# Kernel optimization log

Hardware: AMD Instinct MI355X
Metric: run time of the kernel (lower is better)

The kernel has to match this reference:

```python
import jax, jax.numpy as jnp
import numpy as np

N_NODES = 100000
IN_DIM = 512
OUT_DIM = 16
N_EDGES = 3200000


def setup_inputs() -> dict:
    key = jax.random.key(0)
    k1, k2, k3, k4 = jax.random.split(key, 4)
    x = jax.random.normal(k1, (N_NODES, IN_DIM), dtype=jnp.float32)
    edge_index = jax.random.randint(k2, (2, N_EDGES), 0, N_NODES, dtype=jnp.int64)
    # GCNConv params (glorot weight, zero bias as in PyG)
    scale = jnp.sqrt(6.0 / (IN_DIM + OUT_DIM)).astype(jnp.float32)
    W = jax.random.uniform(k3, (IN_DIM, OUT_DIM), dtype=jnp.float32, minval=-scale, maxval=scale)
    b = jnp.zeros((OUT_DIM,), dtype=jnp.float32)
    return {"x": x, "edge_index": edge_index, "W": W, "b": b}


def reference(x, edge_index, W, b):
    n = x.shape[0]
    # GCNConv with normalize=True: add self-loops, symmetric deg normalization
    loops = jnp.arange(n, dtype=edge_index.dtype)
    row = jnp.concatenate([edge_index[0], loops])  # source nodes
    col = jnp.concatenate([edge_index[1], loops])  # target nodes

    h = x @ W  # [N, 16] dense linear transform

    deg = jax.ops.segment_sum(jnp.ones_like(col, dtype=h.dtype), col, num_segments=n)
    dinv = jnp.where(deg > 0, jax.lax.rsqrt(jnp.maximum(deg, 1.0)), 0.0)
    norm = dinv[row] * dinv[col]  # [E+N]

    # gather source features, scale, scatter-add into targets
    out = jax.ops.segment_sum(norm[:, None] * h[row], col, num_segments=n)
    return out + b
```

## Files before the change

### kernel.cpp

```cpp
#include <hip/hip_runtime.h>
#include <hip/hip_fp16.h>

#define IN_DIM 512
#define OUT_DIM 16
#define KC 32
#define TILE_ROWS 256

#define BSHIFT 8
#define BNODES 256
#define MAXBUCK 512
#define BCOUNT_CHUNK 4096
#define BIN_CHUNK 4096

__global__ __launch_bounds__(256) void gemm_hybrid(const float* __restrict__ x,
                                                   const float* __restrict__ W,
                                                   const int* __restrict__ hist,
                                                   __half* __restrict__ hp, int n) {
    __shared__ float xs[4 * 64 * (KC + 1)];
    const int tid = threadIdx.x;
    const int lane = tid & 63;
    const int w = __builtin_amdgcn_readfirstlane(tid >> 6);
    const int rbase = blockIdx.x * 64;
    const int myrow = rbase + lane;

    float* xw = xs + w * (64 * (KC + 1));
    const int srow = lane >> 3;
    const int scol = (lane & 7) << 2;
    const int kbase = w * 128;

    float4 stA[8], stB[8];

#define LOADC(buf, c)                                                          \
    {                                                                          \
        _Pragma("unroll")                                                      \
        for (int i = 0; i < 8; ++i) {                                          \
            const int rr = rbase + 8 * i + srow;                               \
            if (rr < n)                                                        \
                buf[i] = *(const float4*)(x + (size_t)rr * IN_DIM + kbase + (c) * KC + scol); \
            else                                                               \
                buf[i] = make_float4(0.f, 0.f, 0.f, 0.f);                      \
        }                                                                      \
    }

#define STOREC(buf)                                                            \
    {                                                                          \
        _Pragma("unroll")                                                      \
        for (int i = 0; i < 8; ++i) {                                          \
            float* d = xw + (8 * i + srow) * (KC + 1) + scol;                  \
            d[0] = buf[i].x; d[1] = buf[i].y; d[2] = buf[i].z; d[3] = buf[i].w; \
        }                                                                      \
    }

#define COMPUTEC(c)                                                            \
    {                                                                          \
        const float* xrow = xw + lane * (KC + 1);                              \
        const float* Wb = W + (size_t)(kbase + (c) * KC) * OUT_DIM;            \
        _Pragma("unroll 4")                                                    \
        for (int k = 0; k < KC; ++k) {                                         \
            const float xv = xrow[k];                                          \
            const float* wr = Wb + k * OUT_DIM;                                \
            const float4 w0 = *(const float4*)(wr + 0);                        \
            const float4 w1 = *(const float4*)(wr + 4);                        \
            const float4 w2 = *(const float4*)(wr + 8);                        \
            const float4 w3 = *(const float4*)(wr + 12);                       \
            acc[0]  += xv * w0.x; acc[1]  += xv * w0.y; acc[2]  += xv * w0.z; acc[3]  += xv * w0.w; \
            acc[4]  += xv * w1.x; acc[5]  += xv * w1.y; acc[6]  += xv * w1.z; acc[7]  += xv * w1.w; \
            acc[8]  += xv * w2.x; acc[9]  += xv * w2.y; acc[10] += xv * w2.z; acc[11] += xv * w2.w; \
            acc[12] += xv * w3.x; acc[13] += xv * w3.y; acc[14] += xv * w3.z; acc[15] += xv * w3.w; \
        }                                                                      \
    }

    float acc[OUT_DIM];
#pragma unroll
    for (int j = 0; j < OUT_DIM; ++j) acc[j] = 0.f;

    LOADC(stA, 0);
    STOREC(stA); LOADC(stB, 1); COMPUTEC(0);
    STOREC(stB); LOADC(stA, 2); COMPUTEC(1);
    STOREC(stA); LOADC(stB, 3); COMPUTEC(2);
    STOREC(stB);                COMPUTEC(3);

    __syncthreads();
    if (w > 0) {
        float* d = xs + (w - 1) * (64 * 17) + lane * 17;
#pragma unroll
        for (int j = 0; j < OUT_DIM; ++j) d[j] = acc[j];
    }
    __syncthreads();
    if (tid < 64 && myrow < n) {
        const float* p0 = xs + 0 * (64 * 17) + tid * 17;
        const float* p1 = xs + 1 * (64 * 17) + tid * 17;
        const float* p2 = xs + 2 * (64 * 17) + tid * 17;
        const float s = rsqrtf((float)(hist[myrow] + 1));
        __half2* op = (__half2*)(hp + (size_t)myrow * OUT_DIM);
#pragma unroll
        for (int j = 0; j < 8; ++j) {
            const float lo = acc[2 * j]     + p0[2 * j]     + p1[2 * j]     + p2[2 * j];
            const float hi = acc[2 * j + 1] + p0[2 * j + 1] + p1[2 * j + 1] + p2[2 * j + 1];
            op[j] = __floats2half2_rn(s * lo, s * hi);
        }
    }
#undef LOADC
#undef STOREC
#undef COMPUTEC
}

__global__ __launch_bounds__(256) void gemm_xw(const float* __restrict__ x,
                                               const float* __restrict__ W,
                                               const int* __restrict__ hist,
                                               __half* __restrict__ hp, int n) {
    __shared__ float xs[TILE_ROWS * (KC + 1)];
    const int tid = threadIdx.x;
    const int rbase = blockIdx.x * TILE_ROWS;
    const int myrow = rbase + tid;

    float acc[OUT_DIM];
#pragma unroll
    for (int j = 0; j < OUT_DIM; ++j) acc[j] = 0.f;

    for (int kc = 0; kc < IN_DIM; kc += KC) {
        __syncthreads();
#pragma unroll
        for (int i = 0; i < 8; ++i) {
            const int v = tid + 256 * i;
            const int r = v >> 3;
            const int c = (v & 7) << 2;
            if (rbase + r < n) {
                const float4 f = *(const float4*)(x + (size_t)(rbase + r) * IN_DIM + kc + c);
                float* d = xs + r * (KC + 1) + c;
                d[0] = f.x; d[1] = f.y; d[2] = f.z; d[3] = f.w;
            }
        }
        __syncthreads();

        const float* xrow = xs + tid * (KC + 1);
#pragma unroll 4
        for (int k = 0; k < KC; ++k) {
            const float xv = xrow[k];
            const float* wr = W + (size_t)(kc + k) * OUT_DIM;
            const float4 w0 = *(const float4*)(wr + 0);
            const float4 w1 = *(const float4*)(wr + 4);
            const float4 w2 = *(const float4*)(wr + 8);
            const float4 w3 = *(const float4*)(wr + 12);
            acc[0]  += xv * w0.x; acc[1]  += xv * w0.y; acc[2]  += xv * w0.z; acc[3]  += xv * w0.w;
            acc[4]  += xv * w1.x; acc[5]  += xv * w1.y; acc[6]  += xv * w1.z; acc[7]  += xv * w1.w;
            acc[8]  += xv * w2.x; acc[9]  += xv * w2.y; acc[10] += xv * w2.z; acc[11] += xv * w2.w;
            acc[12] += xv * w3.x; acc[13] += xv * w3.y; acc[14] += xv * w3.z; acc[15] += xv * w3.w;
        }
    }

    if (myrow < n) {
        const float s = rsqrtf((float)(hist[myrow] + 1));
        __half2* op = (__half2*)(hp + (size_t)myrow * OUT_DIM);
#pragma unroll
        for (int j = 0; j < 8; ++j)
            op[j] = __floats2half2_rn(s * acc[2 * j], s * acc[2 * j + 1]);
    }
}

__device__ inline void scan512_excl(const int* src, int* dst, int lane) {
    int c[8], pre[8];
    int tot = 0;
#pragma unroll
    for (int k = 0; k < 8; ++k) { c[k] = src[lane * 8 + k]; pre[k] = tot; tot += c[k]; }
    int incl = tot;
#pragma unroll
    for (int d = 1; d < 64; d <<= 1) {
        const int u = __shfl_up(incl, d);
        if (lane >= d) incl += u;
    }
    const int excl = incl - tot;
#pragma unroll
    for (int k = 0; k < 8; ++k) dst[lane * 8 + k] = excl + pre[k];
}

__device__ inline void scan256_excl(const int* src, int* dst, int lane) {
    int c[4], pre[4];
    int tot = 0;
#pragma unroll
    for (int k = 0; k < 4; ++k) { c[k] = src[lane * 4 + k]; pre[k] = tot; tot += c[k]; }
    int incl = tot;
#pragma unroll
    for (int d = 1; d < 64; d <<= 1) {
        const int u = __shfl_up(incl, d);
        if (lane >= d) incl += u;
    }
    const int excl = incl - tot;
#pragma unroll
    for (int k = 0; k < 4; ++k) dst[lane * 4 + k] = excl + pre[k];
}

__global__ __launch_bounds__(256) void bcount(const int* __restrict__ dst,
                                              int* __restrict__ bcnt, int E, int nbuck) {
    __shared__ int lhist[MAXBUCK];
    const int tid = threadIdx.x;
    for (int i = tid; i < MAXBUCK; i += 256) lhist[i] = 0;
    __syncthreads();

    const int base = blockIdx.x * BCOUNT_CHUNK + tid * 16;
#pragma unroll
    for (int g = 0; g < 4; ++g) {
        const int e = base + g * 4;
        if (e + 3 < E) {
            const int4 d = *(const int4*)(dst + e);
            atomicAdd(&lhist[d.x >> BSHIFT], 1);
            atomicAdd(&lhist[d.y >> BSHIFT], 1);
            atomicAdd(&lhist[d.z >> BSHIFT], 1);
            atomicAdd(&lhist[d.w >> BSHIFT], 1);
        } else {
            for (int u = 0; u < 4; ++u)
                if (e + u < E) atomicAdd(&lhist[dst[e + u] >> BSHIFT], 1);
        }
    }
    __syncthreads();
    for (int i = tid; i < nbuck; i += 256)
        if (lhist[i] > 0) atomicAdd(&bcnt[i], lhist[i]);
}

__global__ __launch_bounds__(512) void bucket_scan(const int* __restrict__ bcnt,
                                                   int* __restrict__ bbase,
                                                   int* __restrict__ bcur, int nbuck) {
    __shared__ int sm[MAXBUCK];
    const int t = threadIdx.x;
    sm[t] = (t < nbuck) ? bcnt[t] : 0;
    __syncthreads();
    if (t < 64) scan512_excl(sm, sm, t);
    __syncthreads();
    bbase[t] = sm[t];
    bcur[t] = sm[t];
}

__global__ __launch_bounds__(256) void bin_edges(const int* __restrict__ ei,
                                                 int* __restrict__ bcur,
                                                 int* __restrict__ bins,
                                                 int E, int nbuck) {
    __shared__ int lhist[MAXBUCK];
    __shared__ int lbase[MAXBUCK];
    __shared__ int gbase[MAXBUCK];
    __shared__ int stage[BIN_CHUNK];
    __shared__ short sbkt[BIN_CHUNK];

    const int tid = threadIdx.x;
    const int e0 = blockIdx.x * BIN_CHUNK;
    const int cnt = min(BIN_CHUNK, E - e0);

    for (int i = tid; i < MAXBUCK; i += 256) lhist[i] = 0;
    __syncthreads();

    int myb[16], myr[16], myp[16];
    const int base = e0 + tid * 16;
#pragma unroll
    for (int g = 0; g < 4; ++g) {
        const int e = base + g * 4;
        int ss[4], dd[4];
        if ((E & 3) == 0 && e + 3 < E) {
            const int4 s4 = *(const int4*)(ei + e);
            const int4 d4 = *(const int4*)(ei + (size_t)E + e);
            ss[0] = s4.x; ss[1] = s4.y; ss[2] = s4.z; ss[3] = s4.w;
            dd[0] = d4.x; dd[1] = d4.y; dd[2] = d4.z; dd[3] = d4.w;
        } else {
#pragma unroll
            for (int u = 0; u < 4; ++u) {
                const int idx = e + u;
                ss[u] = (idx < E) ? ei[idx] : -1;
                dd[u] = (idx < E) ? ei[(size_t)E + idx] : 0;
            }
        }
#pragma unroll
        for (int u = 0; u < 4; ++u) {
            const int j = g * 4 + u;
            if (ss[u] >= 0) {
                const int bk = dd[u] >> BSHIFT;
                myb[j] = bk;
                myp[j] = (ss[u] << BSHIFT) | (dd[u] & (BNODES - 1));
                myr[j] = atomicAdd(&lhist[bk], 1);
            } else {
                myb[j] = -1; myr[j] = 0; myp[j] = 0;
            }
        }
    }
    __syncthreads();

    if (tid < 64) scan512_excl(lhist, lbase, tid);
    for (int i = tid; i < nbuck; i += 256)
        if (lhist[i] > 0) gbase[i] = atomicAdd(&bcur[i], lhist[i]);
    __syncthreads();

#pragma unroll
    for (int j = 0; j < 16; ++j) {
        if (myb[j] >= 0) {
            const int p = lbase[myb[j]] + myr[j];
            stage[p] = myp[j];
            sbkt[p] = (short)myb[j];
        }
    }
    __syncthreads();

    for (int i = tid; i < cnt; i += 256) {
        const int bk = sbkt[i];
        bins[gbase[bk] + (i - lbase[bk])] = stage[i];
    }
}

__global__ __launch_bounds__(1024) void bucket_sort(const int* __restrict__ bins,
                                                    const int* __restrict__ bbase,
                                                    const int* __restrict__ bcur,
                                                    int* __restrict__ csr,
                                                    int* __restrict__ hist,
                                                    int* __restrict__ off, int n) {
    __shared__ int nhist[BNODES];
    __shared__ int nbase[BNODES];
    __shared__ int ncur[BNODES];
    const int tid = threadIdx.x;
    const int b = blockIdx.x;
    const int s = bbase[b];
    const int e = bcur[b];

    if (tid < BNODES) nhist[tid] = 0;
    __syncthreads();
    for (int i = s + tid; i < e; i += 1024)
        atomicAdd(&nhist[bins[i] & (BNODES - 1)], 1);
    __syncthreads();
    if (tid < 64) scan256_excl(nhist, nbase, tid);
    __syncthreads();

    if (tid < BNODES) {
        const int node = (b << BSHIFT) + tid;
        if (node < n) {
            hist[node] = nhist[tid];
            off[node] = s + nbase[tid];
        }
        ncur[tid] = nbase[tid];
    }
    __syncthreads();

    for (int i = s + tid; i < e; i += 1024) {
        const int p = bins[i];
        const int r = atomicAdd(&ncur[p & (BNODES - 1)], 1);
        csr[s + r] = p >> BSHIFT;
    }
}

__global__ __launch_bounds__(256) void gather_out(const int* __restrict__ csr,
                                                  const int* __restrict__ off,
                                                  const int* __restrict__ hist,
                                                  const __half* __restrict__ hp,
                                                  const float* __restrict__ b,
                                                  float* __restrict__ out, int n) {
    const long long gid = (long long)blockIdx.x * 256 + threadIdx.x;
    const int d = (int)(gid >> 3);
    const int j2 = (int)(gid & 7);
    if (d >= n) return;

    const int base = off[d];
    const int deg = hist[d];
    const __half2* hpt = (const __half2*)hp;

    const __half2 sv = hpt[(size_t)d * 8 + j2];
    float ax = __low2float(sv), ay = __high2float(sv);

    int k = 0;
    for (; k + 4 <= deg; k += 4) {
        const int s0 = csr[base + k + 0];
        const int s1 = csr[base + k + 1];
        const int s2 = csr[base + k + 2];
        const int s3 = csr[base + k + 3];
        const __half2 v0 = hpt[(size_t)s0 * 8 + j2];
        const __half2 v1 = hpt[(size_t)s1 * 8 + j2];
        const __half2 v2 = hpt[(size_t)s2 * 8 + j2];
        const __half2 v3 = hpt[(size_t)s3 * 8 + j2];
        ax += __low2float(v0) + __low2float(v1) + __low2float(v2) + __low2float(v3);
        ay += __high2float(v0) + __high2float(v1) + __high2float(v2) + __high2float(v3);
    }
    for (; k < deg; ++k) {
        const __half2 v = hpt[(size_t)csr[base + k] * 8 + j2];
        ax += __low2float(v);
        ay += __high2float(v);
    }

    const float di = rsqrtf((float)(deg + 1));
    float2 o;
    o.x = di * ax + b[2 * j2];
    o.y = di * ay + b[2 * j2 + 1];
    ((float2*)out)[(size_t)d * 8 + j2] = o;
}

__global__ void hist_dst(const int* __restrict__ dst, int* __restrict__ hist, int E) {
    const int t = blockIdx.x * 256 + threadIdx.x;
    const int e0 = t * 4;
    if ((E & 3) == 0 && e0 + 3 < E) {
        const int4 d = *(const int4*)(dst + e0);
        atomicAdd(&hist[d.x], 1);
        atomicAdd(&hist[d.y], 1);
        atomicAdd(&hist[d.z], 1);
        atomicAdd(&hist[d.w], 1);
    } else {
        for (int e = e0; e < E && e < e0 + 4; ++e) atomicAdd(&hist[dst[e]], 1);
    }
}

__global__ __launch_bounds__(256) void scatter_f16(const int* __restrict__ ei,
                                                   const __half* __restrict__ hp,
                                                   __half2* __restrict__ acc, int E) {
    const long long gid = (long long)blockIdx.x * 256 + threadIdx.x;
    const int g = (int)(gid >> 3);
    const int j2 = (int)(gid & 7);
    const int e0 = g * 4;
    if (e0 >= E) return;

    int src[4], dst[4];
#pragma unroll
    for (int u = 0; u < 4; ++u) {
        const int e = e0 + u;
        src[u] = (e < E) ? ei[e] : -1;
        dst[u] = (e < E) ? ei[(size_t)E + e] : -1;
    }
    __half2 v[4];
#pragma unroll
    for (int u = 0; u < 4; ++u)
        if (src[u] >= 0) v[u] = ((const __half2*)(hp + (size_t)src[u] * OUT_DIM))[j2];
#pragma unroll
    for (int u = 0; u < 4; ++u)
        if (dst[u] >= 0) unsafeAtomicAdd(&acc[(size_t)dst[u] * 8 + j2], v[u]);
}

__global__ void finalize(const __half* __restrict__ acc, const __half* __restrict__ hp,
                         const int* __restrict__ hist, const float* __restrict__ b,
                         float* __restrict__ out, int n) {
    const int gid = blockIdx.x * 256 + threadIdx.x;
    if (gid >= n * OUT_DIM) return;
    const int i = gid >> 4;
    const int j = gid & 15;
    const float di = rsqrtf((float)(hist[i] + 1));
    out[gid] = di * (__half2float(acc[gid]) + __half2float(hp[gid])) + b[j];
}


extern "C" void kernel_launch(void* const* d_in, const int* in_sizes, int n_in,
                              void* d_out, int out_size, void* d_ws, size_t ws_size,
                              hipStream_t stream) {
    const float* x  = (const float*)d_in[0];
    const int*   ei = (const int*)d_in[1];
    const float* W  = (const float*)d_in[2];
    const float* b  = (const float*)d_in[3];
    float* out = (float*)d_out;

    const int n = in_sizes[0] / IN_DIM;
    const int E = in_sizes[1] / 2;
    const int nbuck = (n + BNODES - 1) >> BSHIFT;

    __half* hp    = (__half*)d_ws;
    int*    hist  = (int*)(hp + (size_t)n * OUT_DIM);
    int*    off   = hist + n;
    int*    bbase = off + n;
    int*    bcur  = bbase + MAXBUCK;
    int*    bcnt  = bcur + MAXBUCK;
    int*    bins  = bcnt + MAXBUCK;
    int*    csr   = bins + (size_t)E;

    const size_t need = (size_t)n * OUT_DIM * sizeof(__half)
                      + ((size_t)2 * n + 3 * MAXBUCK) * sizeof(int)
                      + 2 * (size_t)E * sizeof(int);

    if (ws_size >= need && nbuck <= MAXBUCK && n < (1 << 23)) {
        hipMemsetAsync(bcnt, 0, MAXBUCK * sizeof(int), stream);

        bcount<<<(E + BCOUNT_CHUNK - 1) / BCOUNT_CHUNK, 256, 0, stream>>>(ei + E, bcnt, E, nbuck);
        bucket_scan<<<1, 512, 0, stream>>>(bcnt, bbase, bcur, nbuck);
        bin_edges<<<(E + BIN_CHUNK - 1) / BIN_CHUNK, 256, 0, stream>>>(ei, bcur, bins, E, nbuck);
        bucket_sort<<<nbuck, 1024, 0, stream>>>(bins, bbase, bcur, csr, hist, off, n);
        gemm_hybrid<<<(n + 63) / 64, 256, 0, stream>>>(x, W, hist, hp, n);
        gather_out<<<(int)(((size_t)n * 8 + 255) / 256), 256, 0, stream>>>(csr, off, hist, hp, b, out, n);
    } else {
        __half* acc = (__half*)(hist + n);
        hipMemsetAsync(hist, 0, (size_t)n * sizeof(int), stream);
        hipMemsetAsync(acc, 0, (size_t)n * OUT_DIM * sizeof(__half), stream);

        hist_dst<<<(E + 1023) / 1024, 256, 0, stream>>>(ei + E, hist, E);
        gemm_xw<<<(n + TILE_ROWS - 1) / TILE_ROWS, 256, 0, stream>>>(x, W, hist, hp, n);
        const long long st = ((long long)(E + 3) / 4) * 8;
        scatter_f16<<<(int)((st + 255) / 256), 256, 0, stream>>>(ei, hp, (__half2*)acc, E);
        finalize<<<(n * OUT_DIM + 255) / 256, 256, 0, stream>>>(acc, hp, hist, b, out, n);
    }
}
```

Before: 401.7 us.

## Load x rows directly into registers in GEMM, dropping LDS staging

Replaces the GEMM's cooperative coalesced load-to-LDS-then-compute scheme with each thread loading its own row slice straight into registers as float4s, double-buffered over eight 16-wide chunks. The aim is to remove LDS stores and reads and the transpose staging. LDS is now used only for the cross-wave reduction. The trade-off is that each lane now reads a separate 2KB-strided row, so global loads are no longer coalesced across lanes, which may raise memory traffic inefficiency on a bandwidth-bound read of x.

```diff
diff --git a/kernel.cpp b/kernel.cpp
--- a/kernel.cpp
+++ b/kernel.cpp
@@ -12,85 +12,80 @@
 #define BCOUNT_CHUNK 4096
 #define BIN_CHUNK 4096
 
-__global__ __launch_bounds__(256) void gemm_hybrid(const float* __restrict__ x,
-                                                   const float* __restrict__ W,
-                                                   const int* __restrict__ hist,
-                                                   __half* __restrict__ hp, int n) {
-    __shared__ float xs[4 * 64 * (KC + 1)];
+__global__ __launch_bounds__(256) void gemm_reg(const float* __restrict__ x,
+                                                const float* __restrict__ W,
+                                                const int* __restrict__ hist,
+                                                __half* __restrict__ hp, int n) {
+    __shared__ float red[3 * 64 * 17];
     const int tid = threadIdx.x;
     const int lane = tid & 63;
     const int w = __builtin_amdgcn_readfirstlane(tid >> 6);
     const int rbase = blockIdx.x * 64;
     const int myrow = rbase + lane;
-
-    float* xw = xs + w * (64 * (KC + 1));
-    const int srow = lane >> 3;
-    const int scol = (lane & 7) << 2;
+    const bool ok = myrow < n;
     const int kbase = w * 128;
 
-    float4 stA[8], stB[8];
-
-#define LOADC(buf, c)                                                          \
+    const float* xr = x + (size_t)myrow * IN_DIM + kbase;
+
+    float acc[OUT_DIM];
+#pragma unroll
+    for (int j = 0; j < OUT_DIM; ++j) acc[j] = 0.f;
+
+    float4 A[4], B[4];
+
+#define LOADR(buf, c)                                                          \
     {                                                                          \
         _Pragma("unroll")                                                      \
-        for (int i = 0; i < 8; ++i) {                                          \
-            const int rr = rbase + 8 * i + srow;                               \
-            if (rr < n)                                                        \
-                buf[i] = *(const float4*)(x + (size_t)rr * IN_DIM + kbase + (c) * KC + scol); \
-            else                                                               \
-                buf[i] = make_float4(0.f, 0.f, 0.f, 0.f);                      \
-        }                                                                      \
-    }
-
-#define STOREC(buf)                                                            \
+        for (int i = 0; i < 4; ++i)                                            \
+            buf[i] = ok ? *(const float4*)(xr + (c) * 16 + i * 4)              \
+                        : make_float4(0.f, 0.f, 0.f, 0.f);                     \
+    }
+
+#define FMA_K(xv, kk)                                                          \
+    {                                                                          \
+        const float* wr = W + (size_t)(kk) * OUT_DIM;    \
+        const float4 w0 = *(const float4*)(wr + 0);                            \
+        const float4 w1 = *(const float4*)(wr + 4);                            \
+        const float4 w2 = *(const float4*)(wr + 8);                            \
+        const float4 w3 = *(const float4*)(wr + 12);                           \
+        acc[0]  += (xv) * w0.x; acc[1]  += (xv) * w0.y; acc[2]  += (xv) * w0.z; acc[3]  += (xv) * w0.w; \
+        acc[4]  += (xv) * w1.x; acc[5]  += (xv) * w1.y; acc[6]  += (xv) * w1.z; acc[7]  += (xv) * w1.w; \
+        acc[8]  += (xv) * w2.x; acc[9]  += (xv) * w2.y; acc[10] += (xv) * w2.z; acc[11] += (xv) * w2.w; \
+        acc[12] += (xv) * w3.x; acc[13] += (xv) * w3.y; acc[14] += (xv) * w3.z; acc[15] += (xv) * w3.w; \
+    }
+
+#define COMPR(buf, c)                                                          \
     {                                                                          \
         _Pragma("unroll")                                                      \
-        for (int i = 0; i < 8; ++i) {                                          \
-            float* d = xw + (8 * i + srow) * (KC + 1) + scol;                  \
-            d[0] = buf[i].x; d[1] = buf[i].y; d[2] = buf[i].z; d[3] = buf[i].w; \
+        for (int i = 0; i < 4; ++i) {                                          \
+            const int k0 = kbase + (c) * 16 + i * 4;                           \
+            FMA_K(buf[i].x, k0 + 0);                                           \
+            FMA_K(buf[i].y, k0 + 1);                                           \
+            FMA_K(buf[i].z, k0 + 2);                                           \
+            FMA_K(buf[i].w, k0 + 3);                                           \
         }                                                                      \
     }
 
-#define COMPUTEC(c)                                                            \
-    {                                                                          \
-        const float* xrow = xw + lane * (KC + 1);                              \
-        const float* Wb = W + (size_t)(kbase + (c) * KC) * OUT_DIM;            \
-        _Pragma("unroll 4")                                                    \
-        for (int k = 0; k < KC; ++k) {                                         \
-            const float xv = xrow[k];                                          \
-            const float* wr = Wb + k * OUT_DIM;                                \
-            const float4 w0 = *(const float4*)(wr + 0);                        \
-            const float4 w1 = *(const float4*)(wr + 4);                        \
-            const float4 w2 = *(const float4*)(wr + 8);                        \
-            const float4 w3 = *(const float4*)(wr + 12);                       \
-            acc[0]  += xv * w0.x; acc[1]  += xv * w0.y; acc[2]  += xv * w0.z; acc[3]  += xv * w0.w; \
-            acc[4]  += xv * w1.x; acc[5]  += xv * w1.y; acc[6]  += xv * w1.z; acc[7]  += xv * w1.w; \
-            acc[8]  += xv * w2.x; acc[9]  += xv * w2.y; acc[10] += xv * w2.z; acc[11] += xv * w2.w; \
-            acc[12] += xv * w3.x; acc[13] += xv * w3.y; acc[14] += xv * w3.z; acc[15] += xv * w3.w; \
-        }                                                                      \
-    }
-
-    float acc[OUT_DIM];
-#pragma unroll
-    for (int j = 0; j < OUT_DIM; ++j) acc[j] = 0.f;
-
-    LOADC(stA, 0);
-    STOREC(stA); LOADC(stB, 1); COMPUTEC(0);
-    STOREC(stB); LOADC(stA, 2); COMPUTEC(1);
-    STOREC(stA); LOADC(stB, 3); COMPUTEC(2);
-    STOREC(stB);                COMPUTEC(3);
-
-    __syncthreads();
+    LOADR(A, 0);
+    LOADR(B, 1); COMPR(A, 0);
+    LOADR(A, 2); COMPR(B, 1);
+    LOADR(B, 3); COMPR(A, 2);
+    LOADR(A, 4); COMPR(B, 3);
+    LOADR(B, 5); COMPR(A, 4);
+    LOADR(A, 6); COMPR(B, 5);
+    LOADR(B, 7); COMPR(A, 6);
+                 COMPR(B, 7);
+
     if (w > 0) {
-        float* d = xs + (w - 1) * (64 * 17) + lane * 17;
+        float* d = red + (w - 1) * (64 * 17) + lane * 17;
 #pragma unroll
         for (int j = 0; j < OUT_DIM; ++j) d[j] = acc[j];
     }
     __syncthreads();
     if (tid < 64 && myrow < n) {
-        const float* p0 = xs + 0 * (64 * 17) + tid * 17;
-        const float* p1 = xs + 1 * (64 * 17) + tid * 17;
-        const float* p2 = xs + 2 * (64 * 17) + tid * 17;
+        const float* p0 = red + 0 * (64 * 17) + tid * 17;
+        const float* p1 = red + 1 * (64 * 17) + tid * 17;
+        const float* p2 = red + 2 * (64 * 17) + tid * 17;
         const float s = rsqrtf((float)(hist[myrow] + 1));
         __half2* op = (__half2*)(hp + (size_t)myrow * OUT_DIM);
 #pragma unroll
@@ -100,9 +95,9 @@
             op[j] = __floats2half2_rn(s * lo, s * hi);
         }
     }
-#undef LOADC
-#undef STOREC
-#undef COMPUTEC
+#undef LOADR
+#undef FMA_K
+#undef COMPR
 }
 
 __global__ __launch_bounds__(256) void gemm_xw(const float* __restrict__ x,
@@ -469,7 +464,7 @@
         bucket_scan<<<1, 512, 0, stream>>>(bcnt, bbase, bcur, nbuck);
         bin_edges<<<(E + BIN_CHUNK - 1) / BIN_CHUNK, 256, 0, stream>>>(ei, bcur, bins, E, nbuck);
         bucket_sort<<<nbuck, 1024, 0, stream>>>(bins, bbase, bcur, csr, hist, off, n);
-        gemm_hybrid<<<(n + 63) / 64, 256, 0, stream>>>(x, W, hist, hp, n);
+        gemm_reg<<<(n + 63) / 64, 256, 0, stream>>>(x, W, hist, hp, n);
         gather_out<<<(int)(((size_t)n * 8 + 255) / 256), 256, 0, stream>>>(csr, off, hist, hp, b, out, n);
     } else {
         __half* acc = (__half*)(hist + n);
```

Result: slower. 617.2 us (+53.6%).
